# Kernel tuning notes

Hardware: AMD Instinct MI355X
Metric: run time of the kernel (lower is better)

The kernel has to match this reference:

```python
import jax, jax.numpy as jnp
import numpy as np

D_MODEL = 512
HEADS = 8
HEAD_DIM = D_MODEL // HEADS


def setup_inputs() -> dict:
    key = jax.random.key(0)
    ks = jax.random.split(key, 6)
    B, T = 4, 2048
    embedding = jax.random.normal(ks[0], (B, T, D_MODEL), dtype=jnp.float32)
    Wq = jax.random.normal(ks[1], (D_MODEL, D_MODEL), dtype=jnp.float32) * 0.02
    Wk = jax.random.normal(ks[2], (D_MODEL, D_MODEL), dtype=jnp.float32) * 0.02
    Wv = jax.random.normal(ks[3], (D_MODEL, D_MODEL), dtype=jnp.float32) * 0.02
    Wo = jax.random.normal(ks[4], (D_MODEL, D_MODEL), dtype=jnp.float32) * 0.02
    bo = jnp.zeros((D_MODEL,), dtype=jnp.float32)
    return {"embedding": embedding, "Wq": Wq, "Wk": Wk, "Wv": Wv, "Wo": Wo, "bo": bo}


def reference(embedding, Wq, Wk, Wv, Wo, bo):
    B, T, _ = embedding.shape
    # nn.Linear (no bias): x @ W.T
    q = embedding @ Wq.T  # [B, T, D]
    v = embedding @ Wv.T
    k = embedding @ Wk.T
    # Faithful to the original: raw reshape (NOT transpose-based head split)
    q = q.reshape(B, HEADS, T, HEAD_DIM)
    k = k.reshape(B, HEADS, T, HEAD_DIM)
    v = v.reshape(B, HEADS, T, HEAD_DIM)
    scores = jnp.einsum('bhqd,bhkd->bhqk', q, k) / jnp.sqrt(jnp.float32(HEAD_DIM))
    # Faithful quirk: softmax over dim=2 (the query axis), as in the source
    attn = jax.nn.softmax(scores, axis=2)
    out = jnp.einsum('bhqk,bhkd->bhqd', attn, v)  # [B, H, T, hd]
    out = out.reshape(B, T, HEADS * HEAD_DIM)  # faithful raw reshape back
    return out @ Wo.T + bo
```

## Files before the change

kernel.cpp:

```cpp
#include <hip/hip_runtime.h>


typedef unsigned short ush;
typedef short s16v8 __attribute__((ext_vector_type(8)));
typedef float f32x4 __attribute__((ext_vector_type(4)));

#define BATCH_STRIDE 1048576
#define HEAD_STRIDE  131072

__device__ __forceinline__ ush f2bf(float f) {
  unsigned int u = __builtin_bit_cast(unsigned int, f);
  u = (u + 0x7FFFu + ((u >> 16) & 1u)) >> 16;
  return (ush)u;
}
__device__ __forceinline__ float bf2f(ush u) {
  return __builtin_bit_cast(float, (unsigned int)u << 16);
}
__device__ __forceinline__ unsigned int bfpack(float lo, float hi) {
  unsigned int ul = __builtin_bit_cast(unsigned int, lo) + 0x8000u;
  unsigned int uh = __builtin_bit_cast(unsigned int, hi) + 0x8000u;
  return (uh & 0xFFFF0000u) | (ul >> 16);
}

__device__ __forceinline__ s16v8 ldsfrag(const ush* base, int row, int ch) {
  return *(const s16v8*)(base + (((row) << 3) + ((ch) ^ ((row) & 7))) * 8);
}

__device__ __forceinline__ f32x4 mfma16(s16v8 a, s16v8 b, f32x4 c) {
  return __builtin_amdgcn_mfma_f32_16x16x32_bf16(a, b, c, 0, 0, 0);
}

__device__ __forceinline__ void gll16(const ush* g, ush* l) {
  __builtin_amdgcn_global_load_lds(
      (const __attribute__((address_space(1))) void*)g,
      (__attribute__((address_space(3))) void*)l, 16, 0, 0);
}

__global__ __launch_bounds__(256) void k_convert(
    const float* __restrict__ X, const float* __restrict__ Wq,
    const float* __restrict__ Wk, const float* __restrict__ Wv,
    const float* __restrict__ Wo, ush* __restrict__ Xb, ush* __restrict__ Wb) {
  int id = blockIdx.x * 256 + threadIdx.x;
  const float* src;
  ush* dst;
  int idx;
  if (id < 1048576) {
    src = X; dst = Xb; idx = id;
  } else {
    int t = id - 1048576;
    int w = t >> 16;
    idx = t & 65535;
    src = (w == 0) ? Wq : (w == 1) ? Wk : (w == 2) ? Wv : Wo;
    dst = Wb + w * 262144;
  }
  float4 v = ((const float4*)src)[idx];
  ushort4 o;
  o.x = f2bf(v.x); o.y = f2bf(v.y); o.z = f2bf(v.z); o.w = f2bf(v.w);
  ((ushort4*)dst)[idx] = o;
}

__device__ __forceinline__ void stage_tile(
    const ush* __restrict__ A, const ush* __restrict__ W,
    ush* lds, int m0, int n0, int k0, int wid, int lane) {
#pragma unroll
  for (int i = 0; i < 4; i++) {
    int s = wid * 4 + i;
    int row = s * 8 + (lane >> 3);
    int ch = (lane & 7) ^ (lane >> 3);
    gll16(A + (size_t)(m0 + row) * 512 + k0 + ch * 8, lds + s * 512);
    gll16(W + (size_t)(n0 + row) * 512 + k0 + ch * 8, lds + 8192 + s * 512);
  }
}

template <int OUTMODE>
__device__ __forceinline__ void gemm2(
    const ush* __restrict__ A, const ush* __restrict__ W,
    ush* __restrict__ Obf, float* __restrict__ Ofp,
    const float* __restrict__ bias, int m0, int n0) {
  __shared__ __align__(16) ush SM[2][16384];
  const int tid = threadIdx.x, lane = tid & 63, wid = tid >> 6;
  const int l16 = lane & 15, lg = lane >> 4;
  const int wr = wid >> 1, wc = wid & 1;

  const f32x4 z4 = {0.f, 0.f, 0.f, 0.f};
  f32x4 acc[4][4];
#pragma unroll
  for (int i = 0; i < 4; i++)
#pragma unroll
    for (int j = 0; j < 4; j++) acc[i][j] = z4;

  stage_tile(A, W, &SM[0][0], m0, n0, 0, wid, lane);
  __syncthreads();
  int cur = 0;
#pragma unroll 1
  for (int t = 0; t < 8; t++) {
    if (t < 7) stage_tile(A, W, &SM[cur ^ 1][0], m0, n0, (t + 1) * 64, wid, lane);
    const ush* At = &SM[cur][0];
    const ush* Bt = &SM[cur][8192];
    s16v8 af[4][2], bf2[4][2];
#pragma unroll
    for (int ms = 0; ms < 4; ms++)
#pragma unroll
      for (int ks = 0; ks < 2; ks++)
        af[ms][ks] = ldsfrag(At, wr * 64 + ms * 16 + l16, ks * 4 + lg);
#pragma unroll
    for (int ns = 0; ns < 4; ns++)
#pragma unroll
      for (int ks = 0; ks < 2; ks++)
        bf2[ns][ks] = ldsfrag(Bt, wc * 64 + ns * 16 + l16, ks * 4 + lg);
#pragma unroll
    for (int ms = 0; ms < 4; ms++)
#pragma unroll
      for (int ns = 0; ns < 4; ns++)
#pragma unroll
        for (int ks = 0; ks < 2; ks++)
          acc[ms][ns] = mfma16(af[ms][ks], bf2[ns][ks], acc[ms][ns]);
    __syncthreads();
    cur ^= 1;
  }

  if (OUTMODE == 0) {
    const int gc0 = n0 + wc * 64;
    const float alpha = (gc0 < 512) ? 0.125f : 1.0f;
    ush* cw = &SM[0][0] + wid * 4096;
#pragma unroll
    for (int ms = 0; ms < 4; ms++)
#pragma unroll
      for (int ns = 0; ns < 4; ns++)
#pragma unroll
        for (int r = 0; r < 4; r++) {
          int row = ms * 16 + lg * 4 + r;
          int col = ns * 16 + l16;
          int sw = (((col >> 3) ^ (row & 7)) << 3) + (col & 7);
          cw[row * 64 + sw] = f2bf(acc[ms][ns][r] * alpha);
        }
    __syncthreads();
    const int z = gc0 >> 9, jl = gc0 & 511;
    ush* og = Obf + (size_t)z * 4194304 + (size_t)(m0 + wr * 64) * 512 + jl;
#pragma unroll
    for (int i = 0; i < 8; i++) {
      int row = i * 8 + (lane >> 3), ch = lane & 7;
      s16v8 v = ldsfrag(cw, row, ch);
      *(s16v8*)(og + (size_t)row * 512 + ch * 8) = v;
    }
  } else {
#pragma unroll
    for (int ms = 0; ms < 4; ms++)
#pragma unroll
      for (int ns = 0; ns < 4; ns++) {
        int gcol = n0 + wc * 64 + ns * 16 + l16;
#pragma unroll
        for (int r = 0; r < 4; r++) {
          int grow = m0 + wr * 64 + ms * 16 + lg * 4 + r;
          Ofp[(size_t)grow * 512 + gcol] = acc[ms][ns][r] + bias[gcol];
        }
      }
  }
}

__global__ __launch_bounds__(256) void k_gemm_qkv(
    const ush* __restrict__ Xb, const ush* __restrict__ Wb,
    ush* __restrict__ QKV) {
  gemm2<0>(Xb, Wb, QKV, nullptr, nullptr, blockIdx.x * 128, blockIdx.y * 128);
}

__global__ __launch_bounds__(256) void k_gemm_out(
    const ush* __restrict__ AO, const ush* __restrict__ Wob,
    float* __restrict__ out, const float* __restrict__ bias) {
  gemm2<1>(AO, Wob, nullptr, out, bias, blockIdx.x * 128, blockIdx.y * 128);
}

__global__ __launch_bounds__(256) void k_colv(
    const ush* __restrict__ Qb, const ush* __restrict__ Kb,
    const ush* __restrict__ Vb, ush* __restrict__ Vst) {
  const int wg = blockIdx.x;
  const int xcd = wg & 7, slot = wg >> 3;
  const int bh = xcd * 4 + (slot >> 5), kt = slot & 31;
  const int b = bh >> 3, h = bh & 7;
  const size_t base = (size_t)b * BATCH_STRIDE + h * HEAD_STRIDE;
  const ush* Qg = Qb + base;
  const ush* Kg = Kb + base + kt * 4096;
  const ush* Vg = Vb + base + kt * 4096;
  ush* dst = Vst + base + kt * 64;

  __shared__ float Zp[256];
  __shared__ float invZ[64];
  __shared__ __align__(16) ush L[64][72];

  const int tid = threadIdx.x, lane = tid & 63, wid = tid >> 6;
  const int l16 = lane & 15, lg = lane >> 4;

  const int cid0 = tid * 2, cid1 = tid * 2 + 1;
  uint4 vr0 = *(const uint4*)(Vg + (size_t)(cid0 >> 3) * 64 + (cid0 & 7) * 8);
  uint4 vr1 = *(const uint4*)(Vg + (size_t)(cid1 >> 3) * 64 + (cid1 & 7) * 8);

  s16v8 kf[4][2];
#pragma unroll
  for (int kc = 0; kc < 4; kc++)
#pragma unroll
    for (int ks = 0; ks < 2; ks++)
      kf[kc][ks] = *(const s16v8*)(Kg + (size_t)(kc * 16 + l16) * 64 + ks * 32 + lg * 8);

  const f32x4 z4 = {0.f, 0.f, 0.f, 0.f};
  f32x4 zacc[4];
#pragma unroll
  for (int kc = 0; kc < 4; kc++) zacc[kc] = z4;

#pragma unroll 1
  for (int t = 0; t < 8; t++) {
    size_t q0 = (size_t)(t * 4 + wid) * 64;
#pragma unroll
    for (int ms = 0; ms < 4; ms++) {
      const ush* qrow = Qg + (q0 + ms * 16 + l16) * 64;
      s16v8 qf0 = *(const s16v8*)(qrow + lg * 8);
      s16v8 qf1 = *(const s16v8*)(qrow + 32 + lg * 8);
#pragma unroll
      for (int kc = 0; kc < 4; kc++) {
        f32x4 s = mfma16(kf[kc][0], qf0, z4);
        s = mfma16(kf[kc][1], qf1, s);
#pragma unroll
        for (int r = 0; r < 4; r++) zacc[kc][r] += __expf(s[r]);
      }
    }
  }

  *(uint4*)(&L[cid0 >> 3][(cid0 & 7) * 8]) = vr0;
  *(uint4*)(&L[cid1 >> 3][(cid1 & 7) * 8]) = vr1;

#pragma unroll
  for (int kc = 0; kc < 4; kc++)
#pragma unroll
    for (int r = 0; r < 4; r++) {
      float v = zacc[kc][r];
      v += __shfl_xor(v, 1); v += __shfl_xor(v, 2);
      v += __shfl_xor(v, 4); v += __shfl_xor(v, 8);
      if (l16 == 0) Zp[wid * 64 + kc * 16 + lg * 4 + r] = v;
    }
  __syncthreads();
  if (tid < 64)
    invZ[tid] = 1.0f / (Zp[tid] + Zp[64 + tid] + Zp[128 + tid] + Zp[192 + tid]);
  __syncthreads();

#pragma unroll
  for (int c = 0; c < 2; c++) {
    int cid = tid * 2 + c, d = cid >> 3, ch = cid & 7;
    float4 iz0 = *(const float4*)(invZ + ch * 8);
    float4 iz1 = *(const float4*)(invZ + ch * 8 + 4);
    ush tmp[8];
#pragma unroll
    for (int j = 0; j < 4; j++) tmp[j] = f2bf(bf2f(L[ch * 8 + j][d]) * iz0[j]);
#pragma unroll
    for (int j = 0; j < 4; j++) tmp[4 + j] = f2bf(bf2f(L[ch * 8 + 4 + j][d]) * iz1[j]);
    *(uint4*)(dst + (size_t)d * 2048 + ch * 8) = *(const uint4*)tmp;
  }
}

__global__ __launch_bounds__(256) void k_attn(
    const ush* __restrict__ Qb, const ush* __restrict__ Kb,
    const ush* __restrict__ Vst, ush* __restrict__ AO) {
  const int wg = blockIdx.x;
  const int xcd = wg & 7, slot = wg >> 3;
  const int bh = xcd * 4 + (slot >> 5), qb = slot & 31;
  const int b = bh >> 3, h = bh & 7;
  const size_t base = (size_t)b * BATCH_STRIDE + h * HEAD_STRIDE;
  const ush* Qg = Qb + base + qb * 4096;
  const ush* Kg = Kb + base;
  const ush* Vg = Vst + base;
  ush* aog = AO + base + qb * 4096;

  __shared__ __align__(16) char smraw[34816];

  const int tid = threadIdx.x, lane = tid & 63, wid = tid >> 6;
  const int l16 = lane & 15, lg = lane >> 4;

  s16v8 qa[4][2];
#pragma unroll
  for (int ms = 0; ms < 4; ms++)
#pragma unroll
    for (int ks = 0; ks < 2; ks++)
      qa[ms][ks] = *(const s16v8*)(Qg + (size_t)(ms * 16 + l16) * 64 + ks * 32 + lg * 8);

  const f32x4 z4 = {0.f, 0.f, 0.f, 0.f};
  f32x4 oacc[4][4];
#pragma unroll
  for (int i = 0; i < 4; i++)
#pragma unroll
    for (int j = 0; j < 4; j++) oacc[i][j] = z4;

  auto stage_v = [&](ush* buf, size_t k0g) {
#pragma unroll
    for (int rd = 0; rd < 4; rd++) {
      int idb = rd * 256 + wid * 64;
      int id = idb + lane;
      int row = id >> 4, sc = id & 15;
      int srcc = (sc & 7) ^ (row & 7);
      gll16(Vg + (size_t)row * 2048 + k0g + ((sc & 8) | srcc) * 8, buf + idb * 8);
    }
  };

  stage_v((ush*)smraw, 0);
  __syncthreads();
  int cur = 0;

  const size_t kwoff = (size_t)(16 * wid + l16) * 64;
#pragma unroll 1
  for (int tp = 0; tp < 16; tp++) {
    if (tp < 15) stage_v((ush*)smraw + (cur ^ 1) * 8192, (size_t)(tp + 1) * 128);
    const ush* Vt = (const ush*)smraw + cur * 8192;

    const ush* kr = Kg + (size_t)tp * 128 * 64 + kwoff;
    s16v8 kf0[2], kf1[2];
    kf0[0] = *(const s16v8*)(kr + lg * 8);
    kf0[1] = *(const s16v8*)(kr + 32 + lg * 8);
    kf1[0] = *(const s16v8*)(kr + 4096 + lg * 8);
    kf1[1] = *(const s16v8*)(kr + 4096 + 32 + lg * 8);

    uint4 vbu[4];
#pragma unroll
    for (int dt = 0; dt < 4; dt++) {
      int row = dt * 16 + l16;
      int cA = 2 * wid + (lg >> 1);
      int offA = row * 128 + (cA ^ (row & 7)) * 8 + (lg & 1) * 4;
      uint2 a = *(const uint2*)(Vt + offA);
      uint2 bq = *(const uint2*)(Vt + offA + 64);
      vbu[dt].x = a.x; vbu[dt].y = a.y; vbu[dt].z = bq.x; vbu[dt].w = bq.y;
    }

#pragma unroll
    for (int ms = 0; ms < 4; ms++) {
      f32x4 sA = mfma16(kf0[0], qa[ms][0], z4);
      sA = mfma16(kf0[1], qa[ms][1], sA);
      f32x4 sB = mfma16(kf1[0], qa[ms][0], z4);
      sB = mfma16(kf1[1], qa[ms][1], sB);
      uint4 pu;
      pu.x = bfpack(__expf(sA[0]), __expf(sA[1]));
      pu.y = bfpack(__expf(sA[2]), __expf(sA[3]));
      pu.z = bfpack(__expf(sB[0]), __expf(sB[1]));
      pu.w = bfpack(__expf(sB[2]), __expf(sB[3]));
      s16v8 pa = __builtin_bit_cast(s16v8, pu);
#pragma unroll
      for (int dt = 0; dt < 4; dt++)
        oacc[ms][dt] = mfma16(pa, __builtin_bit_cast(s16v8, vbu[dt]), oacc[ms][dt]);
    }
    __syncthreads();
    cur ^= 1;
  }

  float* red = (float*)smraw;
  float* r0 = red;
  float* r1 = red + 64 * 68;
  if (wid >= 2) {
    float* rg = (wid == 2) ? r0 : r1;
#pragma unroll
    for (int ms = 0; ms < 4; ms++)
#pragma unroll
      for (int dt = 0; dt < 4; dt++)
        *(f32x4*)(rg + lane * 68 + (ms * 4 + dt) * 4) = oacc[ms][dt];
  }
  __syncthreads();
  if (wid < 2) {
    float* rg = (wid == 0) ? r0 : r1;
#pragma unroll
    for (int ms = 0; ms < 4; ms++)
#pragma unroll
      for (int dt = 0; dt < 4; dt++)
        oacc[ms][dt] += *(const f32x4*)(rg + lane * 68 + (ms * 4 + dt) * 4);
  }
  __syncthreads();
  if (wid == 1) {
#pragma unroll
    for (int ms = 0; ms < 4; ms++)
#pragma unroll
      for (int dt = 0; dt < 4; dt++)
        *(f32x4*)(r0 + lane * 68 + (ms * 4 + dt) * 4) = oacc[ms][dt];
  }
  __syncthreads();
  if (wid == 0) {
#pragma unroll
    for (int ms = 0; ms < 4; ms++)
#pragma unroll
      for (int dt = 0; dt < 4; dt++)
        oacc[ms][dt] += *(const f32x4*)(r0 + lane * 68 + (ms * 4 + dt) * 4);
  }
  __syncthreads();
  ush* ot = (ush*)smraw;
  if (wid == 0) {
#pragma unroll
    for (int ms = 0; ms < 4; ms++)
#pragma unroll
      for (int dt = 0; dt < 4; dt++)
#pragma unroll
        for (int r = 0; r < 4; r++)
          ot[(ms * 16 + lg * 4 + r) * 64 + dt * 16 + l16] = f2bf(oacc[ms][dt][r]);
  }
  __syncthreads();
#pragma unroll
  for (int rd = 0; rd < 2; rd++) {
    int id = rd * 256 + tid;
    *(s16v8*)(aog + id * 8) = *(const s16v8*)(ot + id * 8);
  }
}

extern "C" void kernel_launch(void* const* d_in, const int* in_sizes, int n_in,
                              void* d_out, int out_size, void* d_ws, size_t ws_size,
                              hipStream_t stream) {
  const float* X  = (const float*)d_in[0];
  const float* Wq = (const float*)d_in[1];
  const float* Wk = (const float*)d_in[2];
  const float* Wv = (const float*)d_in[3];
  const float* Wo = (const float*)d_in[4];
  const float* bo = (const float*)d_in[5];

  ush* Qb  = (ush*)d_ws;
  ush* Kb  = Qb + 4194304;
  ush* Vb  = Kb + 4194304;
  ush* Vst = Vb + 4194304;
  ush* AO  = Vst + 4194304;
  ush* Xb  = AO + 4194304;
  ush* Wb  = Xb + 4194304;

  k_convert<<<5120, 256, 0, stream>>>(X, Wq, Wk, Wv, Wo, Xb, Wb);
  k_gemm_qkv<<<dim3(64, 12), 256, 0, stream>>>(Xb, Wb, Qb);
  k_colv<<<1024, 256, 0, stream>>>(Qb, Kb, Vb, Vst);
  k_attn<<<1024, 256, 0, stream>>>(Qb, Kb, Vst, AO);
  k_gemm_out<<<dim3(64, 4), 256, 0, stream>>>(AO, Wb + 3 * 262144, (float*)d_out, bo);
}
```

Baseline: 149.8 us.

## Load V fragments directly from global memory instead of double-buffered LDS staging

After: 180.1 us. +20.3%, slower.

```diff
diff --git a/kernel.cpp b/kernel.cpp
--- a/kernel.cpp
+++ b/kernel.cpp
@@ -268,7 +268,7 @@
   const ush* Vg = Vst + base;
   ush* aog = AO + base + qb * 4096;
 
-  __shared__ __align__(16) char smraw[34816];
+  __shared__ __align__(16) char smraw[32768];
 
   const int tid = threadIdx.x, lane = tid & 63, wid = tid >> 6;
   const int l16 = lane & 15, lg = lane >> 4;
@@ -287,28 +287,11 @@
 #pragma unroll
     for (int j = 0; j < 4; j++) oacc[i][j] = z4;
 
-  auto stage_v = [&](ush* buf, size_t k0g) {
-#pragma unroll
-    for (int rd = 0; rd < 4; rd++) {
-      int idb = rd * 256 + wid * 64;
-      int id = idb + lane;
-      int row = id >> 4, sc = id & 15;
-      int srcc = (sc & 7) ^ (row & 7);
-      gll16(Vg + (size_t)row * 2048 + k0g + ((sc & 8) | srcc) * 8, buf + idb * 8);
-    }
-  };
-
-  stage_v((ush*)smraw, 0);
-  __syncthreads();
-  int cur = 0;
-
-  const size_t kwoff = (size_t)(16 * wid + l16) * 64;
-#pragma unroll 1
+  const ush* krow = Kg + (size_t)(wid * 16 + l16) * 64;
+
+#pragma unroll 2
   for (int tp = 0; tp < 16; tp++) {
-    if (tp < 15) stage_v((ush*)smraw + (cur ^ 1) * 8192, (size_t)(tp + 1) * 128);
-    const ush* Vt = (const ush*)smraw + cur * 8192;
-
-    const ush* kr = Kg + (size_t)tp * 128 * 64 + kwoff;
+    const ush* kr = krow + (size_t)tp * 8192;
     s16v8 kf0[2], kf1[2];
     kf0[0] = *(const s16v8*)(kr + lg * 8);
     kf0[1] = *(const s16v8*)(kr + 32 + lg * 8);
@@ -318,11 +301,10 @@
     uint4 vbu[4];
 #pragma unroll
     for (int dt = 0; dt < 4; dt++) {
-      int row = dt * 16 + l16;
-      int cA = 2 * wid + (lg >> 1);
-      int offA = row * 128 + (cA ^ (row & 7)) * 8 + (lg & 1) * 4;
-      uint2 a = *(const uint2*)(Vt + offA);
-      uint2 bq = *(const uint2*)(Vt + offA + 64);
+      const ush* vp =
+          Vg + (size_t)(dt * 16 + l16) * 2048 + tp * 128 + wid * 16 + lg * 4;
+      uint2 a = *(const uint2*)vp;
+      uint2 bq = *(const uint2*)(vp + 64);
       vbu[dt].x = a.x; vbu[dt].y = a.y; vbu[dt].z = bq.x; vbu[dt].w = bq.y;
     }
 
@@ -342,29 +324,25 @@
       for (int dt = 0; dt < 4; dt++)
         oacc[ms][dt] = mfma16(pa, __builtin_bit_cast(s16v8, vbu[dt]), oacc[ms][dt]);
     }
-    __syncthreads();
-    cur ^= 1;
   }
 
   float* red = (float*)smraw;
-  float* r0 = red;
-  float* r1 = red + 64 * 68;
   if (wid >= 2) {
-    float* rg = (wid == 2) ? r0 : r1;
-#pragma unroll
-    for (int ms = 0; ms < 4; ms++)
-#pragma unroll
-      for (int dt = 0; dt < 4; dt++)
-        *(f32x4*)(rg + lane * 68 + (ms * 4 + dt) * 4) = oacc[ms][dt];
+    float* rg = red + (wid - 2) * 4096;
+#pragma unroll
+    for (int ms = 0; ms < 4; ms++)
+#pragma unroll
+      for (int dt = 0; dt < 4; dt++)
+        *(f32x4*)(rg + (ms * 4 + dt) * 256 + lane * 4) = oacc[ms][dt];
   }
   __syncthreads();
   if (wid < 2) {
-    float* rg = (wid == 0) ? r0 : r1;
-#pragma unroll
-    for (int ms = 0; ms < 4; ms++)
-#pragma unroll
-      for (int dt = 0; dt < 4; dt++)
-        oacc[ms][dt] += *(const f32x4*)(rg + lane * 68 + (ms * 4 + dt) * 4);
+    float* rg = red + wid * 4096;
+#pragma unroll
+    for (int ms = 0; ms < 4; ms++)
+#pragma unroll
+      for (int dt = 0; dt < 4; dt++)
+        oacc[ms][dt] += *(const f32x4*)(rg + (ms * 4 + dt) * 256 + lane * 4);
   }
   __syncthreads();
   if (wid == 1) {
@@ -372,7 +350,7 @@
     for (int ms = 0; ms < 4; ms++)
 #pragma unroll
       for (int dt = 0; dt < 4; dt++)
-        *(f32x4*)(r0 + lane * 68 + (ms * 4 + dt) * 4) = oacc[ms][dt];
+        *(f32x4*)(red + (ms * 4 + dt) * 256 + lane * 4) = oacc[ms][dt];
   }
   __syncthreads();
   if (wid == 0) {
@@ -380,7 +358,7 @@
     for (int ms = 0; ms < 4; ms++)
 #pragma unroll
       for (int dt = 0; dt < 4; dt++)
-        oacc[ms][dt] += *(const f32x4*)(r0 + lane * 68 + (ms * 4 + dt) * 4);
+        oacc[ms][dt] += *(const f32x4*)(red + (ms * 4 + dt) * 256 + lane * 4);
   }
   __syncthreads();
   ush* ot = (ush*)smraw;
```
